# Kernel tuning notes

Hardware: AMD Instinct MI355X
Metric: run time of the kernel (lower is better)

The kernel has to match this reference:

```python
import jax, jax.numpy as jnp
import numpy as np

N, HID, NH = 4096, 1024, 8
D = HID // NH            # ret_size = 128
F_SCALE = 1.0
GAMMA = 1.0 - 2.0 ** (-5)
SCALE_EXP = D ** (-0.5)
LN_EPS = 1e-5


def setup_inputs() -> dict:
    key = jax.random.key(0)
    ks = jax.random.split(key, 12)
    s = HID ** (-0.5)
    return {
        "cur_hiddens": jax.random.normal(ks[0], (N, HID), jnp.float32),
        "f_adj": jax.random.uniform(ks[1], (N, N), jnp.float32),
        "f_dist": jax.random.uniform(ks[2], (N, N), jnp.float32),
        "f_clb": jax.random.normal(ks[3], (N, N), jnp.float32),
        "Wq": jax.random.normal(ks[4], (HID, HID), jnp.float32) * s,
        "Wk": jax.random.normal(ks[5], (HID, HID), jnp.float32) * s,
        "Wv": jax.random.normal(ks[6], (HID, HID), jnp.float32) * s,
        "Wo": jax.random.normal(ks[7], (HID, HID), jnp.float32) * s,
        "bo": jax.random.normal(ks[8], (HID,), jnp.float32) * 0.01,
        "ln_g": jnp.ones((HID,), jnp.float32),
        "ln_b": jnp.zeros((HID,), jnp.float32),
    }


def _layer_norm(x, g, b):
    mu = jnp.mean(x, axis=-1, keepdims=True)
    var = jnp.mean(jnp.square(x - mu), axis=-1, keepdims=True)
    return (x - mu) * jax.lax.rsqrt(var + LN_EPS) * g + b


def reference(cur_hiddens, f_adj, f_dist, f_clb, Wq, Wk, Wv, Wo, bo, ln_g, ln_b):
    n = cur_hiddens.shape[0]
    # projections, reshaped to (heads, atoms, ret_size)
    q = (cur_hiddens @ Wq).reshape(n, NH, D).transpose(1, 0, 2)
    k = (cur_hiddens @ Wk).reshape(n, NH, D).transpose(1, 0, 2)
    v = (cur_hiddens @ Wv).reshape(n, NH, D).transpose(1, 0, 2)
    # retention scores per head: (NH, n, n)
    scores = jnp.einsum('hnd,hmd->hnm', q, k)
    # per-head structural bias injection (no softmax on scores)
    adj_b = F_SCALE * f_adj
    dist_b = F_SCALE * jax.nn.softmax(f_dist, axis=1)
    clb_b = F_SCALE * jax.nn.softmax(f_clb, axis=1)
    scores = scores.at[0].add(adj_b).at[1].add(adj_b)
    scores = scores.at[2].add(dist_b).at[3].add(dist_b)
    scores = scores.at[4].add(clb_b).at[5].add(clb_b)
    scores = scores * (GAMMA ** SCALE_EXP)
    # retention output
    ret = jnp.einsum('hnm,hmd->hnd', scores, v)
    ret = jax.nn.relu(ret)                          # act_func (dropout p=0)
    ret = ret.transpose(1, 0, 2).reshape(n, HID)    # (n, NH*D)
    out = ret @ Wo + bo
    mol_vec = _layer_norm(cur_hiddens + out, ln_g, ln_b)
    return mol_vec, jnp.mean(scores, axis=0)
```

## Files before the change

kernel.cpp:

```cpp
#include <hip/hip_runtime.h>
#include <math.h>

#define NA     4096
#define HID    1024
#define LN_EPS 1e-5f
#define LDSW   40

typedef short s8   __attribute__((ext_vector_type(8)));
typedef float f32x4 __attribute__((ext_vector_type(4)));

#define OFF_XBF   ((size_t)0)
#define OFF_WQT   ((size_t)8<<20)
#define OFF_WKT   ((size_t)10<<20)
#define OFF_WVT   ((size_t)12<<20)
#define OFF_QB    ((size_t)14<<20)
#define OFF_KB    ((size_t)22<<20)
#define OFF_VB    ((size_t)30<<20)
#define OFF_KT    ((size_t)38<<20)
#define OFF_VT    ((size_t)46<<20)
#define OFF_WOT   ((size_t)54<<20)
#define OFF_M2F   ((size_t)56<<20)
#define OFF_M2B   (OFF_M2F + ((size_t)512<<10))
#define OFF_RMAXD (OFF_M2F + ((size_t)768<<10))
#define OFF_RINVD (OFF_RMAXD + 16384)
#define OFF_RMAXC (OFF_RINVD + 16384)
#define OFF_RINVC (OFF_RMAXC + 16384)
#define OFF_RETF  ((size_t)22<<20)
#define OFF_RETB  ((size_t)34<<20)
#define OFF_YF    ((size_t)0)

__device__ __forceinline__ ushort f2bf(float f) {
    unsigned u = __float_as_uint(f);
    u += 0x7FFFu + ((u >> 16) & 1u);
    return (ushort)(u >> 16);
}

__device__ __forceinline__ void mfma_tile(const short* As, const short* Bs,
                                          f32x4 (&acc)[4][4], int lane, int wr, int wc)
{
    const int r = lane & 15, kg = (lane >> 4) * 8;
    s8 a[4], b[4];
#pragma unroll
    for (int i = 0; i < 4; i++) a[i] = *(const s8*)&As[(wr*64 + i*16 + r)*LDSW + kg];
#pragma unroll
    for (int j = 0; j < 4; j++) b[j] = *(const s8*)&Bs[(wc*64 + j*16 + r)*LDSW + kg];
#pragma unroll
    for (int i = 0; i < 4; i++)
#pragma unroll
        for (int j = 0; j < 4; j++)
            acc[i][j] = __builtin_amdgcn_mfma_f32_16x16x32_bf16(a[i], b[j], acc[i][j], 0, 0, 0);
}

__device__ __forceinline__ void gemm_bf16_nt(const ushort* A, int lda,
    const ushort* Bt, int ldb, int K, int row0, int col0,
    short* As, short* Bs, f32x4 (&acc)[4][4], int tid)
{
    const int lane = tid & 63, wave = tid >> 6, wr = wave >> 1, wc = wave & 1;
    const int sr = tid >> 1, sc = (tid & 1) * 16;
    const ushort* Ap = A  + (size_t)(row0 + sr) * lda + sc;
    const ushort* Bp = Bt + (size_t)(col0 + sr) * ldb + sc;
    short* Ad = &As[sr * LDSW + sc];
    short* Bd = &Bs[sr * LDSW + sc];
    for (int kt = 0; kt < K; kt += 32) {
        uint4 a0 = *(const uint4*)(Ap + kt);
        uint4 a1 = *(const uint4*)(Ap + kt + 8);
        uint4 b0 = *(const uint4*)(Bp + kt);
        uint4 b1 = *(const uint4*)(Bp + kt + 8);
        __syncthreads();
        *(uint4*)Ad = a0; *(uint4*)(Ad + 8) = a1;
        *(uint4*)Bd = b0; *(uint4*)(Bd + 8) = b1;
        __syncthreads();
        mfma_tile(As, Bs, acc, lane, wr, wc);
    }
}

#define ZERO_ACC(acc) { f32x4 z = {0.f,0.f,0.f,0.f}; \
    _Pragma("unroll") for (int i=0;i<4;i++) _Pragma("unroll") for (int j=0;j<4;j++) acc[i][j]=z; }

__global__ __launch_bounds__(256) void k_prep(const float* __restrict__ X,
    const float* __restrict__ Wq, const float* __restrict__ Wk,
    const float* __restrict__ Wv, const float* __restrict__ Wo, char* __restrict__ wsb)
{
    const int z = blockIdx.z, bx = blockIdx.x, by = blockIdx.y, t = threadIdx.x;
    const int lr = t >> 2, jb = t & 3;
    if (z == 0) {
        const float* src = X + (size_t)(by*64 + lr) * HID + bx*64 + jb*16;
        ushort* dst = (ushort*)(wsb + OFF_XBF) + (size_t)(by*64 + lr) * HID + bx*64 + jb*16;
        union { ushort u[16]; uint4 q[2]; } pk;
        union { float f[16]; float4 v[4]; } fa;
#pragma unroll
        for (int m = 0; m < 4; m++) fa.v[m] = ((const float4*)src)[m];
#pragma unroll
        for (int m = 0; m < 16; m++) pk.u[m] = f2bf(fa.f[m]);
        ((uint4*)dst)[0] = pk.q[0]; ((uint4*)dst)[1] = pk.q[1];
        return;
    }
    if (by >= 16) return;
    __shared__ ushort Tl[64][72];
    const float* W = (z == 1) ? Wq : (z == 2) ? Wk : (z == 3) ? Wv : Wo;
    ushort* WT = (ushort*)(wsb + ((z==1)?OFF_WQT:(z==2)?OFF_WKT:(z==3)?OFF_WVT:OFF_WOT));
    const int r0 = by*64, c0 = bx*64;
    const float* src = W + (size_t)(r0 + lr) * HID + c0 + jb*16;
    union { float f[16]; float4 v[4]; } fa;
#pragma unroll
    for (int m = 0; m < 4; m++) fa.v[m] = ((const float4*)src)[m];
#pragma unroll
    for (int m = 0; m < 16; m++) Tl[lr][jb*16 + m] = f2bf(fa.f[m]);
    __syncthreads();
    union { ushort u[16]; uint4 q[2]; } pk;
#pragma unroll
    for (int m = 0; m < 16; m++) pk.u[m] = Tl[jb*16 + m][lr];
    ushort* dst = WT + (size_t)(c0 + lr) * HID + r0 + jb*16;
    ((uint4*)dst)[0] = pk.q[0]; ((uint4*)dst)[1] = pk.q[1];
}

__global__ __launch_bounds__(256) void k_rowstats(const float* __restrict__ f_dist,
    const float* __restrict__ f_clb, char* __restrict__ wsb)
{
    const int row = blockIdx.x, mat = blockIdx.y, t = threadIdx.x;
    const float* F = mat ? f_clb : f_dist;
    float* rmax = (float*)(wsb + (mat ? OFF_RMAXC : OFF_RMAXD));
    float* rinv = (float*)(wsb + (mat ? OFF_RINVC : OFF_RINVD));
    float4 v[4];
#pragma unroll
    for (int p = 0; p < 4; p++)
        v[p] = *(const float4*)(F + (size_t)row * NA + 4*t + 1024*p);
    float m = -1e30f;
#pragma unroll
    for (int p = 0; p < 4; p++)
        m = fmaxf(m, fmaxf(fmaxf(v[p].x, v[p].y), fmaxf(v[p].z, v[p].w)));
    for (int off = 32; off; off >>= 1) m = fmaxf(m, __shfl_xor(m, off));
    __shared__ float sb[4];
    if ((t & 63) == 0) sb[t >> 6] = m;
    __syncthreads();
    const float m4 = fmaxf(fmaxf(sb[0], sb[1]), fmaxf(sb[2], sb[3]));
    __syncthreads();
    float s = 0.f;
#pragma unroll
    for (int p = 0; p < 4; p++)
        s += expf(v[p].x-m4) + expf(v[p].y-m4) + expf(v[p].z-m4) + expf(v[p].w-m4);
    for (int off = 32; off; off >>= 1) s += __shfl_xor(s, off);
    if ((t & 63) == 0) sb[t >> 6] = s;
    __syncthreads();
    if (t == 0) { rmax[row] = m4; rinv[row] = 1.0f / (sb[0]+sb[1]+sb[2]+sb[3]); }
}

__global__ __launch_bounds__(256) void k_proj(char* __restrict__ wsb)
{
    __shared__ __align__(16) short As[128*LDSW], Bs[128*LDSW];
    const int z = blockIdx.z;
    const ushort* A  = (const ushort*)(wsb + OFF_XBF);
    const ushort* Bt = (const ushort*)(wsb + ((z==0)?OFF_WQT:(z==1)?OFF_WKT:OFF_WVT));
    ushort* O = (ushort*)(wsb + ((z==0)?OFF_QB:(z==1)?OFF_KB:OFF_VB));
    const int row0 = blockIdx.y*128, col0 = blockIdx.x*128;
    f32x4 acc[4][4]; ZERO_ACC(acc);
    gemm_bf16_nt(A, HID, Bt, HID, HID, row0, col0, As, Bs, acc, threadIdx.x);
    const int lane = threadIdx.x & 63, wave = threadIdx.x >> 6, wr = wave>>1, wc = wave&1;
#pragma unroll
    for (int i = 0; i < 4; i++)
#pragma unroll
    for (int e = 0; e < 4; e++) {
        const int r = row0 + wr*64 + i*16 + (lane>>4)*4 + e;
#pragma unroll
        for (int j = 0; j < 4; j++) {
            const int c = col0 + wc*64 + j*16 + (lane & 15);
            O[(size_t)r*HID + c] = f2bf(acc[i][j][e]);
        }
    }
}

__global__ __launch_bounds__(256) void k_transKV(char* __restrict__ wsb)
{
    const int z = blockIdx.z;
    const ushort* in = (const ushort*)(wsb + (z ? OFF_VB : OFF_KB));
    ushort* out = (ushort*)(wsb + (z ? OFF_VT : OFF_KT));
    const int n0 = blockIdx.y*64, c0 = blockIdx.x*64;
    const int t = threadIdx.x, lr = t >> 2, jb = t & 3;
    __shared__ ushort Tl[64][72];
    const ushort* src = in + (size_t)(n0 + lr) * HID + c0 + jb*16;
    union { ushort u[16]; uint4 q[2]; } pk;
    pk.q[0] = ((const uint4*)src)[0]; pk.q[1] = ((const uint4*)src)[1];
#pragma unroll
    for (int m = 0; m < 16; m++) Tl[lr][jb*16 + m] = pk.u[m];
    __syncthreads();
#pragma unroll
    for (int m = 0; m < 16; m++) pk.u[m] = Tl[jb*16 + m][lr];
    ushort* dst = out + (size_t)(c0 + lr) * NA + n0 + jb*16;
    ((uint4*)dst)[0] = pk.q[0]; ((uint4*)dst)[1] = pk.q[1];
}

__global__ __launch_bounds__(256) void k_ktv(char* __restrict__ wsb)
{
    __shared__ __align__(16) short As[128*LDSW], Bs[128*LDSW];
    const int ci = blockIdx.x, h = blockIdx.y;
    const ushort* A  = (const ushort*)(wsb + OFF_VT) + (size_t)h*128*NA + ci*256;
    const ushort* Bt = (const ushort*)(wsb + OFF_KT) + (size_t)h*128*NA + ci*256;
    f32x4 acc[4][4]; ZERO_ACC(acc);
    gemm_bf16_nt(A, NA, Bt, NA, 256, 0, 0, As, Bs, acc, threadIdx.x);
    float* M2f = (float*)(wsb + OFF_M2F) + (size_t)h*16384;
    const int lane = threadIdx.x & 63, wave = threadIdx.x >> 6, wr = wave>>1, wc = wave&1;
#pragma unroll
    for (int i = 0; i < 4; i++)
#pragma unroll
    for (int e = 0; e < 4; e++) {
        const int r = wr*64 + i*16 + (lane>>4)*4 + e;
#pragma unroll
        for (int j = 0; j < 4; j++) {
            const int c = wc*64 + j*16 + (lane & 15);
            atomicAdd(&M2f[r*128 + c], acc[i][j][e]);
        }
    }
}

__global__ __launch_bounds__(256) void k_m2cvt(char* __restrict__ wsb)
{
    const int i = (blockIdx.x*256 + threadIdx.x) * 8;
    const float* s = (const float*)(wsb + OFF_M2F);
    ushort* d = (ushort*)(wsb + OFF_M2B);
    union { float f[8]; float4 v[2]; } fa;
    fa.v[0] = *(const float4*)(s + i); fa.v[1] = *(const float4*)(s + i + 4);
    union { ushort u[8]; uint4 q; } pk;
#pragma unroll
    for (int m = 0; m < 8; m++) pk.u[m] = f2bf(fa.f[m]);
    *(uint4*)(d + i) = pk.q;
}

__global__ __launch_bounds__(256) void k_scores(char* __restrict__ wsb,
    const float* __restrict__ f_adj, const float* __restrict__ f_dist,
    const float* __restrict__ f_clb, float* __restrict__ outs, float cdiv8, float cdiv4)
{
    __shared__ __align__(16) short As[128*LDSW], Bs[128*LDSW];
    const int row0 = blockIdx.y*128, col0 = blockIdx.x*128;
    f32x4 acc[4][4]; ZERO_ACC(acc);
    gemm_bf16_nt((const ushort*)(wsb + OFF_QB), HID,
                 (const ushort*)(wsb + OFF_KB), HID, HID, row0, col0, As, Bs, acc, threadIdx.x);
    const float* rmaxd = (const float*)(wsb + OFF_RMAXD);
    const float* rinvd = (const float*)(wsb + OFF_RINVD);
    const float* rmaxc = (const float*)(wsb + OFF_RMAXC);
    const float* rinvc = (const float*)(wsb + OFF_RINVC);
    const int lane = threadIdx.x & 63, wave = threadIdx.x >> 6, wr = wave>>1, wc = wave&1;
#pragma unroll
    for (int i = 0; i < 4; i++)
#pragma unroll
    for (int e = 0; e < 4; e++) {
        const int r = row0 + wr*64 + i*16 + (lane>>4)*4 + e;
        const float rmd = rmaxd[r], rid = rinvd[r], rmc = rmaxc[r], ric = rinvc[r];
#pragma unroll
        for (int j = 0; j < 4; j++) {
            const int c = col0 + wc*64 + j*16 + (lane & 15);
            const size_t idx = (size_t)r * NA + c;
            const float bias = f_adj[idx] + __expf(f_dist[idx]-rmd)*rid
                                          + __expf(f_clb[idx]-rmc)*ric;
            outs[idx] = cdiv8 * acc[i][j][e] + cdiv4 * bias;
        }
    }
}

__global__ __launch_bounds__(512, 2) void k_ret2(char* __restrict__ wsb,
    const float* __restrict__ f_adj, const float* __restrict__ f_dist,
    const float* __restrict__ f_clb)
{
    __shared__ __align__(16) short As[128*LDSW];
    __shared__ __align__(16) short Bs[256*LDSW];
    const int kc = blockIdx.x;
    const int row0 = blockIdx.y * 128;
    const int p = blockIdx.z;
    const int tid = threadIdx.x, lane = tid & 63, wave = tid >> 6;
    const int wr = wave >> 2, wc = wave & 3;
    const int ar = tid >> 2, ac = (tid & 3) * 8;
    const int br = tid >> 1, bc = (tid & 1) * 16;

    const float* F = (p == 0) ? f_adj : (p == 1) ? f_dist : f_clb;
    float rm = 0.f, ri = 1.f;
    if (p) {
        rm = ((const float*)(wsb + ((p==1) ? OFF_RMAXD : OFF_RMAXC)))[row0 + ar];
        ri = ((const float*)(wsb + ((p==1) ? OFF_RINVD : OFF_RINVC)))[row0 + ar];
    }
    const float*  Fp = F + (size_t)(row0 + ar) * NA + kc*1024 + ac;
    const ushort* Bp = (const ushort*)(wsb + OFF_VT) + (size_t)(p*256 + br) * NA + kc*1024 + bc;
    short* Ad = &As[ar * LDSW + ac];
    short* Bd = &Bs[br * LDSW + bc];

    f32x4 acc[4][4]; ZERO_ACC(acc);
    for (int kt = 0; kt < 1024; kt += 32) {
        union { float f[8]; float4 v[2]; } fa;
        fa.v[0] = *(const float4*)(Fp + kt);
        fa.v[1] = *(const float4*)(Fp + kt + 4);
        uint4 b0 = *(const uint4*)(Bp + kt);
        uint4 b1 = *(const uint4*)(Bp + kt + 8);
        if (p) {
#pragma unroll
            for (int m = 0; m < 8; m++) fa.f[m] = __expf(fa.f[m] - rm) * ri;
        }
        union { ushort u[8]; uint4 q; } pk;
#pragma unroll
        for (int m = 0; m < 8; m++) pk.u[m] = f2bf(fa.f[m]);
        __syncthreads();
        *(uint4*)Ad = pk.q;
        *(uint4*)Bd = b0; *(uint4*)(Bd + 8) = b1;
        __syncthreads();
        mfma_tile(As, Bs, acc, lane, wr, wc);
    }
    float* RF = (float*)(wsb + OFF_RETF);
#pragma unroll
    for (int i = 0; i < 4; i++)
#pragma unroll
    for (int e = 0; e < 4; e++) {
        const int r = row0 + wr*64 + i*16 + (lane>>4)*4 + e;
#pragma unroll
        for (int j = 0; j < 4; j++) {
            const int c = p*256 + wc*64 + j*16 + (lane & 15);
            atomicAdd(&RF[(size_t)r * 768 + c], acc[i][j][e]);
        }
    }
}

__global__ __launch_bounds__(256) void k_retfin(char* __restrict__ wsb, float c_scale)
{
    __shared__ __align__(16) short As[128*LDSW], Bs[128*LDSW];
    const int h = blockIdx.x, row0 = blockIdx.y * 128;
    const ushort* A  = (const ushort*)(wsb + OFF_QB) + (size_t)row0 * HID + h*128;
    const ushort* Bt = (const ushort*)(wsb + OFF_M2B) + (size_t)h * 16384;
    f32x4 acc[4][4]; ZERO_ACC(acc);
    gemm_bf16_nt(A, HID, Bt, 128, 128, 0, 0, As, Bs, acc, threadIdx.x);
    const float* RF = (const float*)(wsb + OFF_RETF);
    ushort* RB = (ushort*)(wsb + OFF_RETB);
    const int lane = threadIdx.x & 63, wave = threadIdx.x >> 6, wr = wave>>1, wc = wave&1;
#pragma unroll
    for (int i = 0; i < 4; i++)
#pragma unroll
    for (int e = 0; e < 4; e++) {
        const int r = row0 + wr*64 + i*16 + (lane>>4)*4 + e;
#pragma unroll
        for (int j = 0; j < 4; j++) {
            const int cl = wc*64 + j*16 + (lane & 15);
            const int col = h*128 + cl;
            float v = acc[i][j][e];
            if (h < 6) v += RF[(size_t)r * 768 + col];
            RB[(size_t)r * HID + col] = f2bf(fmaxf(c_scale * v, 0.f));
        }
    }
}

__global__ __launch_bounds__(256) void k_wo(char* __restrict__ wsb,
    const float* __restrict__ X, const float* __restrict__ bo)
{
    __shared__ __align__(16) short As[128*LDSW], Bs[128*LDSW];
    const int row0 = blockIdx.y*128, col0 = blockIdx.x*128;
    f32x4 acc[4][4]; ZERO_ACC(acc);
    gemm_bf16_nt((const ushort*)(wsb + OFF_RETB), HID,
                 (const ushort*)(wsb + OFF_WOT), HID, HID, row0, col0, As, Bs, acc, threadIdx.x);
    float* Y = (float*)(wsb + OFF_YF);
    const int lane = threadIdx.x & 63, wave = threadIdx.x >> 6, wr = wave>>1, wc = wave&1;
#pragma unroll
    for (int i = 0; i < 4; i++)
#pragma unroll
    for (int e = 0; e < 4; e++) {
        const int r = row0 + wr*64 + i*16 + (lane>>4)*4 + e;
#pragma unroll
        for (int j = 0; j < 4; j++) {
            const int c = col0 + wc*64 + j*16 + (lane & 15);
            Y[(size_t)r*HID + c] = acc[i][j][e] + X[(size_t)r*HID + c] + bo[c];
        }
    }
}

__global__ __launch_bounds__(256) void k_ln(const char* __restrict__ wsb,
    const float* __restrict__ g, const float* __restrict__ b, float* __restrict__ out)
{
    const float* Y = (const float*)(wsb + OFF_YF);
    const int row = blockIdx.x, t = threadIdx.x;
    float4 v = *(const float4*)(Y + (size_t)row * HID + 4*t);
    float s = v.x + v.y + v.z + v.w;
    for (int off = 32; off; off >>= 1) s += __shfl_xor(s, off);
    __shared__ float sb[4];
    if ((t & 63) == 0) sb[t >> 6] = s;
    __syncthreads();
    const float mu = (sb[0]+sb[1]+sb[2]+sb[3]) * (1.0f / HID);
    const float dx = v.x-mu, dy = v.y-mu, dz = v.z-mu, dw = v.w-mu;
    float q = dx*dx + dy*dy + dz*dz + dw*dw;
    __syncthreads();
    for (int off = 32; off; off >>= 1) q += __shfl_xor(q, off);
    if ((t & 63) == 0) sb[t >> 6] = q;
    __syncthreads();
    const float var = (sb[0]+sb[1]+sb[2]+sb[3]) * (1.0f / HID);
    const float rstd = rsqrtf(var + LN_EPS);
    float4 gv = *(const float4*)(g + 4*t);
    float4 bv = *(const float4*)(b + 4*t);
    float4 o = make_float4(dx*rstd*gv.x + bv.x, dy*rstd*gv.y + bv.y,
                           dz*rstd*gv.z + bv.z, dw*rstd*gv.w + bv.w);
    *(float4*)(out + (size_t)row * HID + 4*t) = o;
}

extern "C" void kernel_launch(void* const* d_in, const int* in_sizes, int n_in,
                              void* d_out, int out_size, void* d_ws, size_t ws_size,
                              hipStream_t stream)
{
    const float* X      = (const float*)d_in[0];
    const float* f_adj  = (const float*)d_in[1];
    const float* f_dist = (const float*)d_in[2];
    const float* f_clb  = (const float*)d_in[3];
    const float* Wq     = (const float*)d_in[4];
    const float* Wk     = (const float*)d_in[5];
    const float* Wv     = (const float*)d_in[6];
    const float* Wo     = (const float*)d_in[7];
    const float* bo     = (const float*)d_in[8];
    const float* ln_g   = (const float*)d_in[9];
    const float* ln_b   = (const float*)d_in[10];

    char* wsb = (char*)d_ws;
    float* out = (float*)d_out;
    float* out_scores = out + (size_t)NA * HID;

    const float c_scale = (float)pow(1.0 - 1.0/32.0, 1.0 / sqrt(128.0));

    hipMemsetAsync(wsb + OFF_M2F, 0, (size_t)512 << 10, stream);

    k_prep    <<<dim3(16, 64, 5), 256, 0, stream>>>(X, Wq, Wk, Wv, Wo, wsb);
    k_rowstats<<<dim3(NA, 2),     256, 0, stream>>>(f_dist, f_clb, wsb);
    k_proj    <<<dim3(8, 32, 3),  256, 0, stream>>>(wsb);
    k_transKV <<<dim3(16, 64, 2), 256, 0, stream>>>(wsb);
    k_ktv     <<<dim3(16, 8),     256, 0, stream>>>(wsb);
    k_m2cvt   <<<64,              256, 0, stream>>>(wsb);
    k_scores  <<<dim3(32, 32),    256, 0, stream>>>(wsb, f_adj, f_dist, f_clb,
                                                    out_scores, c_scale/8.f, c_scale/4.f);
    hipMemsetAsync(wsb + OFF_RETF, 0, (size_t)NA * 768 * 4, stream);
    k_ret2    <<<dim3(4, 32, 3),  512, 0, stream>>>(wsb, f_adj, f_dist, f_clb);
    k_retfin  <<<dim3(8, 32),     256, 0, stream>>>(wsb, c_scale);
    k_wo      <<<dim3(8, 32),     256, 0, stream>>>(wsb, X, bo);
    k_ln      <<<NA,              256, 0, stream>>>(wsb, ln_g, ln_b, out);
}
```

Baseline: 551.6 us.

## Stage GEMM tiles with direct global-to-LDS loads and swizzle score tile order

Replaces register-staged global loads and LDS stores in all GEMM paths with global_load_lds 16-byte direct transfers into an unpadded 32-wide LDS tile layout. The scores kernel also remaps block indices so neighbouring blocks share rows and columns, for better L2 reuse. The goal is to cut VGPR pressure and instruction overhead in the load path. The cost is losing the LDS row padding, which may add bank conflicts in the MFMA fragment reads, and there is still no double buffering.

Result: no change. 544.8 us (-1.2%).

```diff
diff --git a/kernel.cpp b/kernel.cpp
--- a/kernel.cpp
+++ b/kernel.cpp
@@ -4,7 +4,6 @@
 #define NA     4096
 #define HID    1024
 #define LN_EPS 1e-5f
-#define LDSW   40
 
 typedef short s8   __attribute__((ext_vector_type(8)));
 typedef float f32x4 __attribute__((ext_vector_type(4)));
@@ -35,15 +34,21 @@
     return (ushort)(u >> 16);
 }
 
+__device__ __forceinline__ void gl16(const void* g, void* l) {
+    __builtin_amdgcn_global_load_lds(
+        (const __attribute__((address_space(1))) void*)g,
+        (__attribute__((address_space(3))) void*)l, 16, 0, 0);
+}
+
 __device__ __forceinline__ void mfma_tile(const short* As, const short* Bs,
                                           f32x4 (&acc)[4][4], int lane, int wr, int wc)
 {
     const int r = lane & 15, kg = (lane >> 4) * 8;
     s8 a[4], b[4];
 #pragma unroll
-    for (int i = 0; i < 4; i++) a[i] = *(const s8*)&As[(wr*64 + i*16 + r)*LDSW + kg];
-#pragma unroll
-    for (int j = 0; j < 4; j++) b[j] = *(const s8*)&Bs[(wc*64 + j*16 + r)*LDSW + kg];
+    for (int i = 0; i < 4; i++) a[i] = *(const s8*)&As[(wr*64 + i*16 + r)*32 + kg];
+#pragma unroll
+    for (int j = 0; j < 4; j++) b[j] = *(const s8*)&Bs[(wc*64 + j*16 + r)*32 + kg];
 #pragma unroll
     for (int i = 0; i < 4; i++)
 #pragma unroll
@@ -51,24 +56,26 @@
             acc[i][j] = __builtin_amdgcn_mfma_f32_16x16x32_bf16(a[i], b[j], acc[i][j], 0, 0, 0);
 }
 
-__device__ __forceinline__ void gemm_bf16_nt(const ushort* A, int lda,
+__device__ __forceinline__ void gemm_bf16_nt_async(const ushort* A, int lda,
     const ushort* Bt, int ldb, int K, int row0, int col0,
     short* As, short* Bs, f32x4 (&acc)[4][4], int tid)
 {
     const int lane = tid & 63, wave = tid >> 6, wr = wave >> 1, wc = wave & 1;
-    const int sr = tid >> 1, sc = (tid & 1) * 16;
-    const ushort* Ap = A  + (size_t)(row0 + sr) * lda + sc;
-    const ushort* Bp = Bt + (size_t)(col0 + sr) * ldb + sc;
-    short* Ad = &As[sr * LDSW + sc];
-    short* Bd = &Bs[sr * LDSW + sc];
+    const int srow = wave*32 + (lane >> 2), scol = (lane & 3) * 8;
+    const ushort* Ap0 = A  + (size_t)(row0 + srow) * lda + scol;
+    const ushort* Ap1 = Ap0 + 16 * (size_t)lda;
+    const ushort* Bp0 = Bt + (size_t)(col0 + srow) * ldb + scol;
+    const ushort* Bp1 = Bp0 + 16 * (size_t)ldb;
+    short* As0 = As + (wave*32)*32;
+    short* As1 = As + (wave*32+16)*32;
+    short* Bs0 = Bs + (wave*32)*32;
+    short* Bs1 = Bs + (wave*32+16)*32;
     for (int kt = 0; kt < K; kt += 32) {
-        uint4 a0 = *(const uint4*)(Ap + kt);
-        uint4 a1 = *(const uint4*)(Ap + kt + 8);
-        uint4 b0 = *(const uint4*)(Bp + kt);
-        uint4 b1 = *(const uint4*)(Bp + kt + 8);
         __syncthreads();
-        *(uint4*)Ad = a0; *(uint4*)(Ad + 8) = a1;
-        *(uint4*)Bd = b0; *(uint4*)(Bd + 8) = b1;
+        gl16(Ap0 + kt, As0);
+        gl16(Ap1 + kt, As1);
+        gl16(Bp0 + kt, Bs0);
+        gl16(Bp1 + kt, Bs1);
         __syncthreads();
         mfma_tile(As, Bs, acc, lane, wr, wc);
     }
@@ -147,14 +154,14 @@
 
 __global__ __launch_bounds__(256) void k_proj(char* __restrict__ wsb)
 {
-    __shared__ __align__(16) short As[128*LDSW], Bs[128*LDSW];
+    __shared__ __align__(16) short As[128*32], Bs[128*32];
     const int z = blockIdx.z;
     const ushort* A  = (const ushort*)(wsb + OFF_XBF);
     const ushort* Bt = (const ushort*)(wsb + ((z==0)?OFF_WQT:(z==1)?OFF_WKT:OFF_WVT));
     ushort* O = (ushort*)(wsb + ((z==0)?OFF_QB:(z==1)?OFF_KB:OFF_VB));
     const int row0 = blockIdx.y*128, col0 = blockIdx.x*128;
     f32x4 acc[4][4]; ZERO_ACC(acc);
-    gemm_bf16_nt(A, HID, Bt, HID, HID, row0, col0, As, Bs, acc, threadIdx.x);
+    gemm_bf16_nt_async(A, HID, Bt, HID, HID, row0, col0, As, Bs, acc, threadIdx.x);
     const int lane = threadIdx.x & 63, wave = threadIdx.x >> 6, wr = wave>>1, wc = wave&1;
 #pragma unroll
     for (int i = 0; i < 4; i++)
@@ -191,12 +198,12 @@
 
 __global__ __launch_bounds__(256) void k_ktv(char* __restrict__ wsb)
 {
-    __shared__ __align__(16) short As[128*LDSW], Bs[128*LDSW];
+    __shared__ __align__(16) short As[128*32], Bs[128*32];
     const int ci = blockIdx.x, h = blockIdx.y;
     const ushort* A  = (const ushort*)(wsb + OFF_VT) + (size_t)h*128*NA + ci*256;
     const ushort* Bt = (const ushort*)(wsb + OFF_KT) + (size_t)h*128*NA + ci*256;
     f32x4 acc[4][4]; ZERO_ACC(acc);
-    gemm_bf16_nt(A, NA, Bt, NA, 256, 0, 0, As, Bs, acc, threadIdx.x);
+    gemm_bf16_nt_async(A, NA, Bt, NA, 256, 0, 0, As, Bs, acc, threadIdx.x);
     float* M2f = (float*)(wsb + OFF_M2F) + (size_t)h*16384;
     const int lane = threadIdx.x & 63, wave = threadIdx.x >> 6, wr = wave>>1, wc = wave&1;
 #pragma unroll
@@ -229,11 +236,14 @@
     const float* __restrict__ f_adj, const float* __restrict__ f_dist,
     const float* __restrict__ f_clb, float* __restrict__ outs, float cdiv8, float cdiv4)
 {
-    __shared__ __align__(16) short As[128*LDSW], Bs[128*LDSW];
-    const int row0 = blockIdx.y*128, col0 = blockIdx.x*128;
-    f32x4 acc[4][4]; ZERO_ACC(acc);
-    gemm_bf16_nt((const ushort*)(wsb + OFF_QB), HID,
-                 (const ushort*)(wsb + OFF_KB), HID, HID, row0, col0, As, Bs, acc, threadIdx.x);
+    __shared__ __align__(16) short As[128*32], Bs[128*32];
+    const int lin = blockIdx.y*32 + blockIdx.x;
+    const int sw  = (lin & 7)*128 + (lin >> 3);
+    const int row0 = (sw >> 5)*128, col0 = (sw & 31)*128;
+    f32x4 acc[4][4]; ZERO_ACC(acc);
+    gemm_bf16_nt_async((const ushort*)(wsb + OFF_QB), HID,
+                       (const ushort*)(wsb + OFF_KB), HID, HID, row0, col0,
+                       As, Bs, acc, threadIdx.x);
     const float* rmaxd = (const float*)(wsb + OFF_RMAXD);
     const float* rinvd = (const float*)(wsb + OFF_RINVD);
     const float* rmaxc = (const float*)(wsb + OFF_RMAXC);
@@ -260,15 +270,15 @@
     const float* __restrict__ f_adj, const float* __restrict__ f_dist,
     const float* __restrict__ f_clb)
 {
-    __shared__ __align__(16) short As[128*LDSW];
-    __shared__ __align__(16) short Bs[256*LDSW];
+    __shared__ __align__(16) short As[128*32];
+    __shared__ __align__(16) short Bs[256*32];
     const int kc = blockIdx.x;
     const int row0 = blockIdx.y * 128;
     const int p = blockIdx.z;
     const int tid = threadIdx.x, lane = tid & 63, wave = tid >> 6;
     const int wr = wave >> 2, wc = wave & 3;
     const int ar = tid >> 2, ac = (tid & 3) * 8;
-    const int br = tid >> 1, bc = (tid & 1) * 16;
+    const int srow = wave*32 + (lane >> 2), scol = (lane & 3) * 8;
 
     const float* F = (p == 0) ? f_adj : (p == 1) ? f_dist : f_clb;
     float rm = 0.f, ri = 1.f;
@@ -276,18 +286,18 @@
         rm = ((const float*)(wsb + ((p==1) ? OFF_RMAXD : OFF_RMAXC)))[row0 + ar];
         ri = ((const float*)(wsb + ((p==1) ? OFF_RINVD : OFF_RINVC)))[row0 + ar];
     }
-    const float*  Fp = F + (size_t)(row0 + ar) * NA + kc*1024 + ac;
-    const ushort* Bp = (const ushort*)(wsb + OFF_VT) + (size_t)(p*256 + br) * NA + kc*1024 + bc;
-    short* Ad = &As[ar * LDSW + ac];
-    short* Bd = &Bs[br * LDSW + bc];
+    const float*  Fp  = F + (size_t)(row0 + ar) * NA + kc*1024 + ac;
+    const ushort* Bp0 = (const ushort*)(wsb + OFF_VT) + (size_t)(p*256 + srow) * NA + kc*1024 + scol;
+    const ushort* Bp1 = Bp0 + 16 * (size_t)NA;
+    short* Ad  = &As[ar * 32 + ac];
+    short* Bs0 = &Bs[(wave*32)*32];
+    short* Bs1 = &Bs[(wave*32+16)*32];
 
     f32x4 acc[4][4]; ZERO_ACC(acc);
     for (int kt = 0; kt < 1024; kt += 32) {
         union { float f[8]; float4 v[2]; } fa;
         fa.v[0] = *(const float4*)(Fp + kt);
         fa.v[1] = *(const float4*)(Fp + kt + 4);
-        uint4 b0 = *(const uint4*)(Bp + kt);
-        uint4 b1 = *(const uint4*)(Bp + kt + 8);
         if (p) {
 #pragma unroll
             for (int m = 0; m < 8; m++) fa.f[m] = __expf(fa.f[m] - rm) * ri;
@@ -296,8 +306,9 @@
 #pragma unroll
         for (int m = 0; m < 8; m++) pk.u[m] = f2bf(fa.f[m]);
         __syncthreads();
+        gl16(Bp0 + kt, Bs0);
+        gl16(Bp1 + kt, Bs1);
         *(uint4*)Ad = pk.q;
-        *(uint4*)Bd = b0; *(uint4*)(Bd + 8) = b1;
         __syncthreads();
         mfma_tile(As, Bs, acc, lane, wr, wc);
     }
@@ -317,12 +328,12 @@
 
 __global__ __launch_bounds__(256) void k_retfin(char* __restrict__ wsb, float c_scale)
 {
-    __shared__ __align__(16) short As[128*LDSW], Bs[128*LDSW];
+    __shared__ __align__(16) short As[128*32], Bs[128*32];
     const int h = blockIdx.x, row0 = blockIdx.y * 128;
     const ushort* A  = (const ushort*)(wsb + OFF_QB) + (size_t)row0 * HID + h*128;
     const ushort* Bt = (const ushort*)(wsb + OFF_M2B) + (size_t)h * 16384;
     f32x4 acc[4][4]; ZERO_ACC(acc);
-    gemm_bf16_nt(A, HID, Bt, 128, 128, 0, 0, As, Bs, acc, threadIdx.x);
+    gemm_bf16_nt_async(A, HID, Bt, 128, 128, 0, 0, As, Bs, acc, threadIdx.x);
     const float* RF = (const float*)(wsb + OFF_RETF);
     ushort* RB = (ushort*)(wsb + OFF_RETB);
     const int lane = threadIdx.x & 63, wave = threadIdx.x >> 6, wr = wave>>1, wc = wave&1;
@@ -345,11 +356,12 @@
 __global__ __launch_bounds__(256) void k_wo(char* __restrict__ wsb,
     const float* __restrict__ X, const float* __restrict__ bo)
 {
-    __shared__ __align__(16) short As[128*LDSW], Bs[128*LDSW];
+    __shared__ __align__(16) short As[128*32], Bs[128*32];
     const int row0 = blockIdx.y*128, col0 = blockIdx.x*128;
     f32x4 acc[4][4]; ZERO_ACC(acc);
-    gemm_bf16_nt((const ushort*)(wsb + OFF_RETB), HID,
-                 (const ushort*)(wsb + OFF_WOT), HID, HID, row0, col0, As, Bs, acc, threadIdx.x);
+    gemm_bf16_nt_async((const ushort*)(wsb + OFF_RETB), HID,
+                       (const ushort*)(wsb + OFF_WOT), HID, HID, row0, col0,
+                       As, Bs, acc, threadIdx.x);
     float* Y = (float*)(wsb + OFF_YF);
     const int lane = threadIdx.x & 63, wave = threadIdx.x >> 6, wr = wave>>1, wc = wave&1;
 #pragma unroll
```
